# Performance work log

Measured on AMD Instinct MI355X. Metric: run time of the kernel, lower is better.

Reference implementation:

```python
import jax, jax.numpy as jnp
import numpy as np

# ---- sRGB <-> CIELAB (D65) helpers, matching standard torch lab2rgb/rgb2lab ----
_RGB2XYZ = jnp.array([[0.412453, 0.357580, 0.180423],
                      [0.212671, 0.715160, 0.072169],
                      [0.019334, 0.119193, 0.950227]], dtype=jnp.float32)
_XYZ2RGB = jnp.array([[ 3.2404542, -1.5371385, -0.4985314],
                      [-0.9692660,  1.8760108,  0.0415560],
                      [ 0.0556434, -0.2040259,  1.0572252]], dtype=jnp.float32)
_WHITE = jnp.array([0.95047, 1.0, 1.08883], dtype=jnp.float32)
_EPS = 0.008856      # (6/29)^3
_KAPPA = 7.787

def _srgb_to_linear(c):
    safe = jnp.maximum(c, 0.04045)
    return jnp.where(c <= 0.04045, c / 12.92, ((safe + 0.055) / 1.055) ** 2.4)

def _linear_to_srgb(c):
    safe = jnp.maximum(c, 0.0031308)
    return jnp.where(c <= 0.0031308, 12.92 * c, 1.055 * safe ** (1.0 / 2.4) - 0.055)

def rgb2lab(rgb):
    lin = _srgb_to_linear(rgb)                      # [N,3]
    xyz = (lin @ _RGB2XYZ.T) / _WHITE               # [N,3]
    safe = jnp.maximum(xyz, _EPS)
    f = jnp.where(xyz > _EPS, jnp.cbrt(safe), _KAPPA * xyz + 16.0 / 116.0)
    fx, fy, fz = f[..., 0], f[..., 1], f[..., 2]
    L = 116.0 * fy - 16.0
    a = 500.0 * (fx - fy)
    b = 200.0 * (fy - fz)
    return jnp.stack([L, a, b], axis=-1)

def lab2rgb(lab):
    L, a, b = lab[..., 0], lab[..., 1], lab[..., 2]
    fy = (L + 16.0) / 116.0
    fx = fy + a / 500.0
    fz = fy - b / 200.0
    f = jnp.stack([fx, fy, fz], axis=-1)
    f3 = f ** 3
    t = jnp.where(f3 > _EPS, f3, (f - 16.0 / 116.0) / _KAPPA)
    xyz = t * _WHITE
    lin = xyz @ _XYZ2RGB.T
    return _linear_to_srgb(lin)

def _forward(x, w_seq1, b_seq1, w_seq2, b_seq2, w_lin, b_lin,
             w_comb, b_comb, w_logd, b_logd, w_final, b_final):
    # lab branch
    seq = jnp.tanh(x @ w_seq1 + b_seq1) @ w_seq2 + b_seq2        # [N,3]
    lin = x @ w_lin + b_lin                                      # [N,3]
    final_lab = jnp.concatenate([lin, seq], axis=-1) @ w_comb + b_comb
    # log-density branch
    x_rgb = lab2rgb(x)
    log_density = -jnp.log10(x_rgb)
    model_processed = log_density @ w_logd + b_logd
    back_to_lab = rgb2lab(10.0 ** model_processed)
    return jnp.concatenate([final_lab, back_to_lab], axis=-1) @ w_final + b_final


def setup_inputs() -> dict:
    key = jax.random.key(0)
    ks = jax.random.split(key, 13)
    N, H = 2_097_152, 64

    def lin_init(kw, kb, fan_in, fan_out):
        bound = 1.0 / np.sqrt(fan_in)
        w = jax.random.uniform(kw, (fan_in, fan_out), minval=-bound, maxval=bound, dtype=jnp.float32)
        b = jax.random.uniform(kb, (fan_out,), minval=-bound, maxval=bound, dtype=jnp.float32)
        return w, b

    # valid Lab inputs: sample sRGB away from 0/1 then convert
    rgb = jax.random.uniform(ks[0], (N, 3), minval=0.05, maxval=0.95, dtype=jnp.float32)
    x = rgb2lab(rgb)

    kk = jax.random.split(ks[1], 12)
    w_seq1, b_seq1 = lin_init(kk[0], kk[1], 3, H)
    w_seq2, b_seq2 = lin_init(kk[2], kk[3], H, 3)
    w_lin, b_lin = lin_init(kk[4], kk[5], 3, 3)
    w_comb, b_comb = lin_init(kk[6], kk[7], 6, 3)
    w_logd, b_logd = lin_init(kk[8], kk[9], 3, 3)
    w_final, b_final = lin_init(kk[10], kk[11], 6, 3)
    return {"x": x,
            "w_seq1": w_seq1, "b_seq1": b_seq1, "w_seq2": w_seq2, "b_seq2": b_seq2,
            "w_lin": w_lin, "b_lin": b_lin, "w_comb": w_comb, "b_comb": b_comb,
            "w_logd": w_logd, "b_logd": b_logd, "w_final": w_final, "b_final": b_final}


def reference(x, w_seq1, b_seq1, w_seq2, b_seq2, w_lin, b_lin,
              w_comb, b_comb, w_logd, b_logd, w_final, b_final):
    return _forward(x, w_seq1, b_seq1, w_seq2, b_seq2, w_lin, b_lin,
                    w_comb, b_comb, w_logd, b_logd, w_final, b_final)
```

## Files before the change

kernel.cpp:

```cpp
#include <hip/hip_runtime.h>

typedef float    v2f __attribute__((ext_vector_type(2)));
typedef _Float16 v2h __attribute__((ext_vector_type(2)));

__device__ __forceinline__ float fexp2(float x) { return __builtin_amdgcn_exp2f(x); }
__device__ __forceinline__ float flog2(float x) { return __builtin_amdgcn_logf(x); }
__device__ __forceinline__ float ffma (float a, float b, float c) { return __builtin_fmaf(a, b, c); }
__device__ __forceinline__ v2f  splat(float s) { v2f v; v.x = s; v.y = s; return v; }
__device__ __forceinline__ v2f  pkfma(v2f a, v2f b, v2f c) { return __builtin_elementwise_fma(a, b, c); }
__device__ __forceinline__ v2h  splath(float s) { v2h v; v.x = (_Float16)s; v.y = (_Float16)s; return v; }
__device__ __forceinline__ v2h  pkfmah(v2h a, v2h b, v2h c) { return __builtin_elementwise_fma(a, b, c); }
__device__ __forceinline__ v2h  cvt_pk(float a, float b) {
    return __builtin_bit_cast(v2h, __builtin_amdgcn_cvt_pkrtz(a, b));
}

#define LAB_EPS 0.008856f
#define F16_116 0.13793103448275862f
#define LOG2_10 3.3219280948873623f

__device__ __align__(16) float g_ws[548];

__global__ __launch_bounds__(64) void prep_kernel(
    const float* __restrict__ w_seq1, const float* __restrict__ b_seq1,
    const float* __restrict__ w_seq2, const float* __restrict__ b_seq2,
    const float* __restrict__ w_lin,  const float* __restrict__ b_lin,
    const float* __restrict__ w_comb, const float* __restrict__ b_comb,
    const float* __restrict__ w_logd, const float* __restrict__ b_logd,
    const float* __restrict__ w_final,const float* __restrict__ b_final)
{
    const int j = threadIdx.x;
    float H3[9];
#pragma unroll
    for (int i = 0; i < 3; ++i)
#pragma unroll
        for (int c = 0; c < 3; ++c) {
            float h = 0.f;
            for (int m = 0; m < 3; ++m) h += w_comb[(i + 3) * 3 + m] * w_final[m * 3 + c];
            H3[i * 3 + c] = h;
        }

    float4* wsa = reinterpret_cast<float4*>(g_ws);
    uint4*  wsb = reinterpret_cast<uint4*>(g_ws) + 64;

    wsa[j] = make_float4(w_seq1[j], w_seq1[64 + j], w_seq1[128 + j], b_seq1[j]);
    const float w0 = w_seq2[j * 3 + 0], w1 = w_seq2[j * 3 + 1], w2 = w_seq2[j * 3 + 2];
    const float wp0 = w0 * H3[0] + w1 * H3[3] + w2 * H3[6];
    const float wp1 = w0 * H3[1] + w1 * H3[4] + w2 * H3[7];
    const float wp2 = w0 * H3[2] + w1 * H3[5] + w2 * H3[8];
    uint4 wb;
    wb.x = __builtin_bit_cast(unsigned, cvt_pk(wp0, wp0));
    wb.y = __builtin_bit_cast(unsigned, cvt_pk(wp1, wp1));
    wb.z = __builtin_bit_cast(unsigned, cvt_pk(wp2, wp2));
    wb.w = 0u;
    wsb[j] = wb;

    if (j == 0) {
        float* sm = g_ws + 512;
        float G[9], Wfb[9];
#pragma unroll
        for (int i = 0; i < 3; ++i)
#pragma unroll
            for (int c = 0; c < 3; ++c) {
                float gg = 0.f;
                for (int m = 0; m < 3; ++m) gg += w_comb[i * 3 + m] * w_final[m * 3 + c];
                G[i * 3 + c] = gg;
            }
#pragma unroll
        for (int k = 0; k < 3; ++k)
#pragma unroll
            for (int c = 0; c < 3; ++c) {
                float s = 0.f;
                for (int i = 0; i < 3; ++i) s += w_lin[k * 3 + i] * G[i * 3 + c];
                sm[k * 3 + c]      = s;
                Wfb[k * 3 + c]     = w_final[(k + 3) * 3 + c];
                sm[18 + k * 3 + c] = -w_logd[k * 3 + c];
            }
#pragma unroll
        for (int c = 0; c < 3; ++c) {
            sm[9 + c]     = 500.0f * Wfb[3 + c];
            sm[9 + 3 + c] = 116.0f * Wfb[c] - 500.0f * Wfb[3 + c] + 200.0f * Wfb[6 + c];
            sm[9 + 6 + c] = -200.0f * Wfb[6 + c];
            float s = b_final[c] - 16.0f * Wfb[c];
            for (int i = 0; i < 3; ++i)
                s += b_lin[i] * G[i * 3 + c] + b_seq2[i] * H3[i * 3 + c]
                   + b_comb[i] * w_final[i * 3 + c];
            sm[27 + c] = LOG2_10 * b_logd[c];
            sm[30 + c] = s;
        }
    }
}

__global__ __launch_bounds__(256, 5) void fused_kernel(
    const float* __restrict__ x,
    float* __restrict__ out, int n)
{
    const float4* __restrict__ wsa = reinterpret_cast<const float4*>(g_ws);
    const uint4*  __restrict__ wsb = reinterpret_cast<const uint4*>(g_ws) + 64;
    const float*  __restrict__ wse = g_ws + 512;

    const int g = blockIdx.x * blockDim.x + threadIdx.x;
    if (g * 2 >= n) return;

    const float2* xin = reinterpret_cast<const float2*>(x) + (size_t)g * 3;
    const float2 v0 = xin[0], v1 = xin[1], v2 = xin[2];
    v2f xs2[3];
    xs2[0].x = v0.x; xs2[0].y = v1.y;
    xs2[1].x = v0.y; xs2[1].y = v2.x;
    xs2[2].x = v1.x; xs2[2].y = v2.y;

    v2h acc0 = splath(0.f), acc1 = splath(0.f), acc2 = splath(0.f);

#pragma unroll 2
    for (int j0 = 0; j0 < 64; j0 += 4) {
        float4 wa0 = wsa[j0 + 0], wa1 = wsa[j0 + 1], wa2 = wsa[j0 + 2], wa3 = wsa[j0 + 3];
        uint4  wb0 = wsb[j0 + 0], wb1 = wsb[j0 + 1], wb2 = wsb[j0 + 2], wb3 = wsb[j0 + 3];

        v2f t0 = pkfma(xs2[0], splat(wa0.x), pkfma(xs2[1], splat(wa0.y), pkfma(xs2[2], splat(wa0.z), splat(wa0.w))));
        v2f t1 = pkfma(xs2[0], splat(wa1.x), pkfma(xs2[1], splat(wa1.y), pkfma(xs2[2], splat(wa1.z), splat(wa1.w))));
        v2f t2 = pkfma(xs2[0], splat(wa2.x), pkfma(xs2[1], splat(wa2.y), pkfma(xs2[2], splat(wa2.z), splat(wa2.w))));
        v2f t3 = pkfma(xs2[0], splat(wa3.x), pkfma(xs2[1], splat(wa3.y), pkfma(xs2[2], splat(wa3.z), splat(wa3.w))));

        v2h th0 = cvt_pk(t0.x, t0.y);
        v2h th1 = cvt_pk(t1.x, t1.y);
        v2h th2 = cvt_pk(t2.x, t2.y);
        v2h th3 = cvt_pk(t3.x, t3.y);

        const v2h hi3 = splath(3.0f), lo3 = splath(-3.0f);
        th0 = __builtin_elementwise_min(__builtin_elementwise_max(th0, lo3), hi3);
        th1 = __builtin_elementwise_min(__builtin_elementwise_max(th1, lo3), hi3);
        th2 = __builtin_elementwise_min(__builtin_elementwise_max(th2, lo3), hi3);
        th3 = __builtin_elementwise_min(__builtin_elementwise_max(th3, lo3), hi3);

        v2h u0 = th0 * th0, u1 = th1 * th1, u2 = th2 * th2, u3 = th3 * th3;

        const v2h c3 = splath(-0.00120984f), c2 = splath(0.02603622f);
        const v2h c1 = splath(-0.20598500f), c0 = splath(0.95858467f);
        v2h P0 = pkfmah(c3, u0, c2);
        v2h P1 = pkfmah(c3, u1, c2);
        v2h P2 = pkfmah(c3, u2, c2);
        v2h P3 = pkfmah(c3, u3, c2);
        P0 = pkfmah(P0, u0, c1);
        P1 = pkfmah(P1, u1, c1);
        P2 = pkfmah(P2, u2, c1);
        P3 = pkfmah(P3, u3, c1);
        P0 = pkfmah(P0, u0, c0);
        P1 = pkfmah(P1, u1, c0);
        P2 = pkfmah(P2, u2, c0);
        P3 = pkfmah(P3, u3, c0);

        v2h h0 = th0 * P0, h1 = th1 * P1, h2 = th2 * P2, h3 = th3 * P3;

        acc0 = pkfmah(h0, __builtin_bit_cast(v2h, wb0.x), acc0);
        acc1 = pkfmah(h0, __builtin_bit_cast(v2h, wb0.y), acc1);
        acc2 = pkfmah(h0, __builtin_bit_cast(v2h, wb0.z), acc2);
        acc0 = pkfmah(h1, __builtin_bit_cast(v2h, wb1.x), acc0);
        acc1 = pkfmah(h1, __builtin_bit_cast(v2h, wb1.y), acc1);
        acc2 = pkfmah(h1, __builtin_bit_cast(v2h, wb1.z), acc2);
        acc0 = pkfmah(h2, __builtin_bit_cast(v2h, wb2.x), acc0);
        acc1 = pkfmah(h2, __builtin_bit_cast(v2h, wb2.y), acc1);
        acc2 = pkfmah(h2, __builtin_bit_cast(v2h, wb2.z), acc2);
        acc0 = pkfmah(h3, __builtin_bit_cast(v2h, wb3.x), acc0);
        acc1 = pkfmah(h3, __builtin_bit_cast(v2h, wb3.y), acc1);
        acc2 = pkfmah(h3, __builtin_bit_cast(v2h, wb3.z), acc2);
    }

    float A[9], U[9], Wn[9], bl2[3], cv[3];
#pragma unroll
    for (int i = 0; i < 9; ++i) { A[i] = wse[i]; U[i] = wse[9 + i]; Wn[i] = wse[18 + i]; }
#pragma unroll
    for (int i = 0; i < 3; ++i) { bl2[i] = wse[27 + i]; cv[i] = wse[30 + i]; }

    float ov[6];
#pragma unroll
    for (int p = 0; p < 2; ++p) {
        const float L  = p ? xs2[0].y : xs2[0].x;
        const float aa = p ? xs2[1].y : xs2[1].x;
        const float bb = p ? xs2[2].y : xs2[2].x;
        const float a0 = p ? (float)acc0.y : (float)acc0.x;
        const float a1 = p ? (float)acc1.y : (float)acc1.x;
        const float a2 = p ? (float)acc2.y : (float)acc2.x;
        const float fy = (L + 16.0f) * (1.0f / 116.0f);
        const float fx = ffma(aa,  0.002f, fy);
        const float fz = ffma(bb, -0.005f, fy);
        float rgb[3];
        {
            const float f3x = fx * fx * fx, f3y = fy * fy * fy, f3z = fz * fz * fz;
            const float tx = f3x > LAB_EPS ? f3x : (fx - F16_116) * (1.0f / 7.787f);
            const float ty = f3y > LAB_EPS ? f3y : (fy - F16_116) * (1.0f / 7.787f);
            const float tz = f3z > LAB_EPS ? f3z : (fz - F16_116) * (1.0f / 7.787f);
            const float X = tx * 0.95047f, Y = ty, Z = tz * 1.08883f;
            const float linv[3] = {
                 3.2404542f * X - 1.5371385f * Y - 0.4985314f * Z,
                -0.9692660f * X + 1.8760108f * Y + 0.0415560f * Z,
                 0.0556434f * X - 0.2040259f * Y + 1.0572252f * Z};
#pragma unroll
            for (int c = 0; c < 3; ++c) {
                const float cc = linv[c];
                const float lo = 12.92f * cc;
                const float hi = ffma(1.055f,
                                      fexp2(flog2(fmaxf(cc, 0.0031308f)) * (1.0f / 2.4f)),
                                      -0.055f);
                rgb[c] = cc <= 0.0031308f ? lo : hi;
            }
        }
        const float lg0 = flog2(rgb[0]);
        const float lg1 = flog2(rgb[1]);
        const float lg2 = flog2(rgb[2]);
        float lin2[3];
#pragma unroll
        for (int c = 0; c < 3; ++c) {
            const float e   = ffma(lg0, Wn[c], ffma(lg1, Wn[3 + c], ffma(lg2, Wn[6 + c], bl2[c])));
            const float r10 = fexp2(e);
            const float lo  = r10 * (1.0f / 12.92f);
            const float base = (fmaxf(r10, 0.04045f) + 0.055f) * (1.0f / 1.055f);
            const float hi  = fexp2(2.4f * flog2(base));
            lin2[c] = r10 <= 0.04045f ? lo : hi;
        }
        const float X2 = (0.412453f * lin2[0] + 0.357580f * lin2[1] + 0.180423f * lin2[2]) * (1.0f / 0.95047f);
        const float Y2 =  0.212671f * lin2[0] + 0.715160f * lin2[1] + 0.072169f * lin2[2];
        const float Z2 = (0.019334f * lin2[0] + 0.119193f * lin2[1] + 0.950227f * lin2[2]) * (1.0f / 1.08883f);
        const float fX = X2 > LAB_EPS ? fexp2(flog2(fmaxf(X2, LAB_EPS)) * (1.0f / 3.0f)) : ffma(7.787f, X2, F16_116);
        const float fY = Y2 > LAB_EPS ? fexp2(flog2(fmaxf(Y2, LAB_EPS)) * (1.0f / 3.0f)) : ffma(7.787f, Y2, F16_116);
        const float fZ = Z2 > LAB_EPS ? fexp2(flog2(fmaxf(Z2, LAB_EPS)) * (1.0f / 3.0f)) : ffma(7.787f, Z2, F16_116);
#pragma unroll
        for (int c = 0; c < 3; ++c) {
            float o = cv[c];
            o = ffma(L,  A[c],     o);
            o = ffma(aa, A[3 + c], o);
            o = ffma(bb, A[6 + c], o);
            o += (c == 0 ? a0 : (c == 1 ? a1 : a2));
            o = ffma(fX, U[c],     o);
            o = ffma(fY, U[3 + c], o);
            o = ffma(fZ, U[6 + c], o);
            ov[p * 3 + c] = o;
        }
    }

    float2* op = reinterpret_cast<float2*>(out) + (size_t)g * 3;
    op[0] = make_float2(ov[0], ov[1]);
    op[1] = make_float2(ov[2], ov[3]);
    op[2] = make_float2(ov[4], ov[5]);
}

extern "C" void kernel_launch(void* const* d_in, const int* in_sizes, int n_in,
                              void* d_out, int out_size, void* d_ws, size_t ws_size,
                              hipStream_t stream)
{
    const float* x       = (const float*)d_in[0];
    const float* w_seq1  = (const float*)d_in[1];
    const float* b_seq1  = (const float*)d_in[2];
    const float* w_seq2  = (const float*)d_in[3];
    const float* b_seq2  = (const float*)d_in[4];
    const float* w_lin   = (const float*)d_in[5];
    const float* b_lin   = (const float*)d_in[6];
    const float* w_comb  = (const float*)d_in[7];
    const float* b_comb  = (const float*)d_in[8];
    const float* w_logd  = (const float*)d_in[9];
    const float* b_logd  = (const float*)d_in[10];
    const float* w_final = (const float*)d_in[11];
    const float* b_final = (const float*)d_in[12];
    float* outp = (float*)d_out;

    const int n = in_sizes[0] / 3;
    const int threads = 256;
    const int total_threads = (n + 1) / 2;
    const int blocks = (total_threads + threads - 1) / threads;

    prep_kernel<<<1, 64, 0, stream>>>(
        w_seq1, b_seq1, w_seq2, b_seq2, w_lin, b_lin, w_comb, b_comb,
        w_logd, b_logd, w_final, b_final);
    fused_kernel<<<blocks, threads, 0, stream>>>(x, outp, n);
}
```

Before: 138.1 us.

## Fold weight prep into main kernel via LDS and pack color tail math

Removes the separate prep kernel launch by having each block compute the folded weights into shared memory before a barrier. The first-layer weights are now read directly from the original input layout as float4 rows. The color-space tail is rewritten to process both points per thread with packed float2 arithmetic instead of a scalar loop over two points. The cost is redundant per-block weight folding plus a __syncthreads, and launch bounds drop the occupancy hint.

```diff
diff --git a/kernel.cpp b/kernel.cpp
--- a/kernel.cpp
+++ b/kernel.cpp
@@ -13,92 +13,92 @@
 __device__ __forceinline__ v2h  cvt_pk(float a, float b) {
     return __builtin_bit_cast(v2h, __builtin_amdgcn_cvt_pkrtz(a, b));
 }
+__device__ __forceinline__ v2f pexp2(v2f e) { v2f r; r.x = fexp2(e.x); r.y = fexp2(e.y); return r; }
+__device__ __forceinline__ v2f plog2(v2f e) { v2f r; r.x = flog2(e.x); r.y = flog2(e.y); return r; }
+__device__ __forceinline__ v2f selgt(v2f c, float thr, v2f a, v2f b) {
+    v2f r; r.x = c.x > thr ? a.x : b.x; r.y = c.y > thr ? a.y : b.y; return r;
+}
+__device__ __forceinline__ v2f selle(v2f c, float thr, v2f a, v2f b) {
+    v2f r; r.x = c.x <= thr ? a.x : b.x; r.y = c.y <= thr ? a.y : b.y; return r;
+}
+__device__ __forceinline__ v2f pmax(v2f a, float s) { return __builtin_elementwise_max(a, splat(s)); }
 
 #define LAB_EPS 0.008856f
 #define F16_116 0.13793103448275862f
 #define LOG2_10 3.3219280948873623f
 
-__device__ __align__(16) float g_ws[548];
-
-__global__ __launch_bounds__(64) void prep_kernel(
+__global__ __launch_bounds__(256) void fused_kernel(
+    const float* __restrict__ x,
     const float* __restrict__ w_seq1, const float* __restrict__ b_seq1,
     const float* __restrict__ w_seq2, const float* __restrict__ b_seq2,
     const float* __restrict__ w_lin,  const float* __restrict__ b_lin,
     const float* __restrict__ w_comb, const float* __restrict__ b_comb,
     const float* __restrict__ w_logd, const float* __restrict__ b_logd,
-    const float* __restrict__ w_final,const float* __restrict__ b_final)
-{
-    const int j = threadIdx.x;
-    float H3[9];
-#pragma unroll
-    for (int i = 0; i < 3; ++i)
-#pragma unroll
-        for (int c = 0; c < 3; ++c) {
-            float h = 0.f;
-            for (int m = 0; m < 3; ++m) h += w_comb[(i + 3) * 3 + m] * w_final[m * 3 + c];
-            H3[i * 3 + c] = h;
-        }
-
-    float4* wsa = reinterpret_cast<float4*>(g_ws);
-    uint4*  wsb = reinterpret_cast<uint4*>(g_ws) + 64;
-
-    wsa[j] = make_float4(w_seq1[j], w_seq1[64 + j], w_seq1[128 + j], b_seq1[j]);
-    const float w0 = w_seq2[j * 3 + 0], w1 = w_seq2[j * 3 + 1], w2 = w_seq2[j * 3 + 2];
-    const float wp0 = w0 * H3[0] + w1 * H3[3] + w2 * H3[6];
-    const float wp1 = w0 * H3[1] + w1 * H3[4] + w2 * H3[7];
-    const float wp2 = w0 * H3[2] + w1 * H3[5] + w2 * H3[8];
-    uint4 wb;
-    wb.x = __builtin_bit_cast(unsigned, cvt_pk(wp0, wp0));
-    wb.y = __builtin_bit_cast(unsigned, cvt_pk(wp1, wp1));
-    wb.z = __builtin_bit_cast(unsigned, cvt_pk(wp2, wp2));
-    wb.w = 0u;
-    wsb[j] = wb;
-
-    if (j == 0) {
-        float* sm = g_ws + 512;
-        float G[9], Wfb[9];
-#pragma unroll
-        for (int i = 0; i < 3; ++i)
-#pragma unroll
-            for (int c = 0; c < 3; ++c) {
-                float gg = 0.f;
-                for (int m = 0; m < 3; ++m) gg += w_comb[i * 3 + m] * w_final[m * 3 + c];
-                G[i * 3 + c] = gg;
-            }
-#pragma unroll
-        for (int k = 0; k < 3; ++k)
-#pragma unroll
-            for (int c = 0; c < 3; ++c) {
-                float s = 0.f;
-                for (int i = 0; i < 3; ++i) s += w_lin[k * 3 + i] * G[i * 3 + c];
-                sm[k * 3 + c]      = s;
-                Wfb[k * 3 + c]     = w_final[(k + 3) * 3 + c];
-                sm[18 + k * 3 + c] = -w_logd[k * 3 + c];
-            }
-#pragma unroll
-        for (int c = 0; c < 3; ++c) {
-            sm[9 + c]     = 500.0f * Wfb[3 + c];
-            sm[9 + 3 + c] = 116.0f * Wfb[c] - 500.0f * Wfb[3 + c] + 200.0f * Wfb[6 + c];
-            sm[9 + 6 + c] = -200.0f * Wfb[6 + c];
-            float s = b_final[c] - 16.0f * Wfb[c];
-            for (int i = 0; i < 3; ++i)
-                s += b_lin[i] * G[i * 3 + c] + b_seq2[i] * H3[i * 3 + c]
-                   + b_comb[i] * w_final[i * 3 + c];
-            sm[27 + c] = LOG2_10 * b_logd[c];
-            sm[30 + c] = s;
-        }
-    }
-}
-
-__global__ __launch_bounds__(256, 5) void fused_kernel(
-    const float* __restrict__ x,
+    const float* __restrict__ w_final,const float* __restrict__ b_final,
     float* __restrict__ out, int n)
 {
-    const float4* __restrict__ wsa = reinterpret_cast<const float4*>(g_ws);
-    const uint4*  __restrict__ wsb = reinterpret_cast<const uint4*>(g_ws) + 64;
-    const float*  __restrict__ wse = g_ws + 512;
-
-    const int g = blockIdx.x * blockDim.x + threadIdx.x;
+    __shared__ uint4 wsbL[64];
+    __shared__ float smlds[33];
+
+    const int tid = threadIdx.x;
+    if (tid < 64) {
+        const int j = tid;
+        float H3[9];
+#pragma unroll
+        for (int i = 0; i < 3; ++i)
+#pragma unroll
+            for (int c = 0; c < 3; ++c) {
+                float h = 0.f;
+                for (int m = 0; m < 3; ++m) h += w_comb[(i + 3) * 3 + m] * w_final[m * 3 + c];
+                H3[i * 3 + c] = h;
+            }
+        const float w0 = w_seq2[j * 3 + 0], w1 = w_seq2[j * 3 + 1], w2 = w_seq2[j * 3 + 2];
+        const float wp0 = w0 * H3[0] + w1 * H3[3] + w2 * H3[6];
+        const float wp1 = w0 * H3[1] + w1 * H3[4] + w2 * H3[7];
+        const float wp2 = w0 * H3[2] + w1 * H3[5] + w2 * H3[8];
+        uint4 wb;
+        wb.x = __builtin_bit_cast(unsigned, cvt_pk(wp0, wp0));
+        wb.y = __builtin_bit_cast(unsigned, cvt_pk(wp1, wp1));
+        wb.z = __builtin_bit_cast(unsigned, cvt_pk(wp2, wp2));
+        wb.w = 0u;
+        wsbL[j] = wb;
+        if (j == 0) {
+            float G[9], Wfb[9];
+#pragma unroll
+            for (int i = 0; i < 3; ++i)
+#pragma unroll
+                for (int c = 0; c < 3; ++c) {
+                    float gg = 0.f;
+                    for (int m = 0; m < 3; ++m) gg += w_comb[i * 3 + m] * w_final[m * 3 + c];
+                    G[i * 3 + c] = gg;
+                }
+#pragma unroll
+            for (int k = 0; k < 3; ++k)
+#pragma unroll
+                for (int c = 0; c < 3; ++c) {
+                    float s = 0.f;
+                    for (int i = 0; i < 3; ++i) s += w_lin[k * 3 + i] * G[i * 3 + c];
+                    smlds[k * 3 + c]      = s;
+                    Wfb[k * 3 + c]        = w_final[(k + 3) * 3 + c];
+                    smlds[18 + k * 3 + c] = -w_logd[k * 3 + c];
+                }
+#pragma unroll
+            for (int c = 0; c < 3; ++c) {
+                smlds[9 + c]     = 500.0f * Wfb[3 + c];
+                smlds[9 + 3 + c] = 116.0f * Wfb[c] - 500.0f * Wfb[3 + c] + 200.0f * Wfb[6 + c];
+                smlds[9 + 6 + c] = -200.0f * Wfb[6 + c];
+                float s = b_final[c] - 16.0f * Wfb[c];
+                for (int i = 0; i < 3; ++i)
+                    s += b_lin[i] * G[i * 3 + c] + b_seq2[i] * H3[i * 3 + c]
+                       + b_comb[i] * w_final[i * 3 + c];
+                smlds[27 + c] = LOG2_10 * b_logd[c];
+                smlds[30 + c] = s;
+            }
+        }
+    }
+    __syncthreads();
+
+    const int g = blockIdx.x * blockDim.x + tid;
     if (g * 2 >= n) return;
 
     const float2* xin = reinterpret_cast<const float2*>(x) + (size_t)g * 3;
@@ -110,15 +110,22 @@
 
     v2h acc0 = splath(0.f), acc1 = splath(0.f), acc2 = splath(0.f);
 
+    const float4* __restrict__ w1v = reinterpret_cast<const float4*>(w_seq1);
+    const float4* __restrict__ b1v = reinterpret_cast<const float4*>(b_seq1);
+
 #pragma unroll 2
     for (int j0 = 0; j0 < 64; j0 += 4) {
-        float4 wa0 = wsa[j0 + 0], wa1 = wsa[j0 + 1], wa2 = wsa[j0 + 2], wa3 = wsa[j0 + 3];
-        uint4  wb0 = wsb[j0 + 0], wb1 = wsb[j0 + 1], wb2 = wsb[j0 + 2], wb3 = wsb[j0 + 3];
-
-        v2f t0 = pkfma(xs2[0], splat(wa0.x), pkfma(xs2[1], splat(wa0.y), pkfma(xs2[2], splat(wa0.z), splat(wa0.w))));
-        v2f t1 = pkfma(xs2[0], splat(wa1.x), pkfma(xs2[1], splat(wa1.y), pkfma(xs2[2], splat(wa1.z), splat(wa1.w))));
-        v2f t2 = pkfma(xs2[0], splat(wa2.x), pkfma(xs2[1], splat(wa2.y), pkfma(xs2[2], splat(wa2.z), splat(wa2.w))));
-        v2f t3 = pkfma(xs2[0], splat(wa3.x), pkfma(xs2[1], splat(wa3.y), pkfma(xs2[2], splat(wa3.z), splat(wa3.w))));
+        const int q = j0 >> 2;
+        const float4 wr0 = w1v[q];
+        const float4 wr1 = w1v[16 + q];
+        const float4 wr2 = w1v[32 + q];
+        const float4 wrb = b1v[q];
+        const uint4 wb0 = wsbL[j0 + 0], wb1 = wsbL[j0 + 1], wb2 = wsbL[j0 + 2], wb3 = wsbL[j0 + 3];
+
+        v2f t0 = pkfma(xs2[0], splat(wr0.x), pkfma(xs2[1], splat(wr1.x), pkfma(xs2[2], splat(wr2.x), splat(wrb.x))));
+        v2f t1 = pkfma(xs2[0], splat(wr0.y), pkfma(xs2[1], splat(wr1.y), pkfma(xs2[2], splat(wr2.y), splat(wrb.y))));
+        v2f t2 = pkfma(xs2[0], splat(wr0.z), pkfma(xs2[1], splat(wr1.z), pkfma(xs2[2], splat(wr2.z), splat(wrb.z))));
+        v2f t3 = pkfma(xs2[0], splat(wr0.w), pkfma(xs2[1], splat(wr1.w), pkfma(xs2[2], splat(wr2.w), splat(wrb.w))));
 
         v2h th0 = cvt_pk(t0.x, t0.y);
         v2h th1 = cvt_pk(t1.x, t1.y);
@@ -166,80 +173,72 @@
 
     float A[9], U[9], Wn[9], bl2[3], cv[3];
 #pragma unroll
-    for (int i = 0; i < 9; ++i) { A[i] = wse[i]; U[i] = wse[9 + i]; Wn[i] = wse[18 + i]; }
-#pragma unroll
-    for (int i = 0; i < 3; ++i) { bl2[i] = wse[27 + i]; cv[i] = wse[30 + i]; }
-
-    float ov[6];
-#pragma unroll
-    for (int p = 0; p < 2; ++p) {
-        const float L  = p ? xs2[0].y : xs2[0].x;
-        const float aa = p ? xs2[1].y : xs2[1].x;
-        const float bb = p ? xs2[2].y : xs2[2].x;
-        const float a0 = p ? (float)acc0.y : (float)acc0.x;
-        const float a1 = p ? (float)acc1.y : (float)acc1.x;
-        const float a2 = p ? (float)acc2.y : (float)acc2.x;
-        const float fy = (L + 16.0f) * (1.0f / 116.0f);
-        const float fx = ffma(aa,  0.002f, fy);
-        const float fz = ffma(bb, -0.005f, fy);
-        float rgb[3];
-        {
-            const float f3x = fx * fx * fx, f3y = fy * fy * fy, f3z = fz * fz * fz;
-            const float tx = f3x > LAB_EPS ? f3x : (fx - F16_116) * (1.0f / 7.787f);
-            const float ty = f3y > LAB_EPS ? f3y : (fy - F16_116) * (1.0f / 7.787f);
-            const float tz = f3z > LAB_EPS ? f3z : (fz - F16_116) * (1.0f / 7.787f);
-            const float X = tx * 0.95047f, Y = ty, Z = tz * 1.08883f;
-            const float linv[3] = {
-                 3.2404542f * X - 1.5371385f * Y - 0.4985314f * Z,
-                -0.9692660f * X + 1.8760108f * Y + 0.0415560f * Z,
-                 0.0556434f * X - 0.2040259f * Y + 1.0572252f * Z};
-#pragma unroll
-            for (int c = 0; c < 3; ++c) {
-                const float cc = linv[c];
-                const float lo = 12.92f * cc;
-                const float hi = ffma(1.055f,
-                                      fexp2(flog2(fmaxf(cc, 0.0031308f)) * (1.0f / 2.4f)),
-                                      -0.055f);
-                rgb[c] = cc <= 0.0031308f ? lo : hi;
-            }
-        }
-        const float lg0 = flog2(rgb[0]);
-        const float lg1 = flog2(rgb[1]);
-        const float lg2 = flog2(rgb[2]);
-        float lin2[3];
-#pragma unroll
-        for (int c = 0; c < 3; ++c) {
-            const float e   = ffma(lg0, Wn[c], ffma(lg1, Wn[3 + c], ffma(lg2, Wn[6 + c], bl2[c])));
-            const float r10 = fexp2(e);
-            const float lo  = r10 * (1.0f / 12.92f);
-            const float base = (fmaxf(r10, 0.04045f) + 0.055f) * (1.0f / 1.055f);
-            const float hi  = fexp2(2.4f * flog2(base));
-            lin2[c] = r10 <= 0.04045f ? lo : hi;
-        }
-        const float X2 = (0.412453f * lin2[0] + 0.357580f * lin2[1] + 0.180423f * lin2[2]) * (1.0f / 0.95047f);
-        const float Y2 =  0.212671f * lin2[0] + 0.715160f * lin2[1] + 0.072169f * lin2[2];
-        const float Z2 = (0.019334f * lin2[0] + 0.119193f * lin2[1] + 0.950227f * lin2[2]) * (1.0f / 1.08883f);
-        const float fX = X2 > LAB_EPS ? fexp2(flog2(fmaxf(X2, LAB_EPS)) * (1.0f / 3.0f)) : ffma(7.787f, X2, F16_116);
-        const float fY = Y2 > LAB_EPS ? fexp2(flog2(fmaxf(Y2, LAB_EPS)) * (1.0f / 3.0f)) : ffma(7.787f, Y2, F16_116);
-        const float fZ = Z2 > LAB_EPS ? fexp2(flog2(fmaxf(Z2, LAB_EPS)) * (1.0f / 3.0f)) : ffma(7.787f, Z2, F16_116);
-#pragma unroll
-        for (int c = 0; c < 3; ++c) {
-            float o = cv[c];
-            o = ffma(L,  A[c],     o);
-            o = ffma(aa, A[3 + c], o);
-            o = ffma(bb, A[6 + c], o);
-            o += (c == 0 ? a0 : (c == 1 ? a1 : a2));
-            o = ffma(fX, U[c],     o);
-            o = ffma(fY, U[3 + c], o);
-            o = ffma(fZ, U[6 + c], o);
-            ov[p * 3 + c] = o;
-        }
+    for (int i = 0; i < 9; ++i) { A[i] = smlds[i]; U[i] = smlds[9 + i]; Wn[i] = smlds[18 + i]; }
+#pragma unroll
+    for (int i = 0; i < 3; ++i) { bl2[i] = smlds[27 + i]; cv[i] = smlds[30 + i]; }
+
+    v2f sq0, sq1, sq2;
+    sq0.x = (float)acc0.x; sq0.y = (float)acc0.y;
+    sq1.x = (float)acc1.x; sq1.y = (float)acc1.y;
+    sq2.x = (float)acc2.x; sq2.y = (float)acc2.y;
+
+    const v2f fy = (xs2[0] + splat(16.0f)) * splat(1.0f / 116.0f);
+    const v2f fx = pkfma(xs2[1], splat( 0.002f), fy);
+    const v2f fz = pkfma(xs2[2], splat(-0.005f), fy);
+    const v2f f3x = fx * fx * fx, f3y = fy * fy * fy, f3z = fz * fz * fz;
+    const v2f tx = selgt(f3x, LAB_EPS, f3x, (fx - splat(F16_116)) * splat(1.0f / 7.787f));
+    const v2f ty = selgt(f3y, LAB_EPS, f3y, (fy - splat(F16_116)) * splat(1.0f / 7.787f));
+    const v2f tz = selgt(f3z, LAB_EPS, f3z, (fz - splat(F16_116)) * splat(1.0f / 7.787f));
+    const v2f X = tx * splat(0.95047f), Y = ty, Z = tz * splat(1.08883f);
+    v2f linv[3];
+    linv[0] = pkfma(X, splat( 3.2404542f), pkfma(Y, splat(-1.5371385f), Z * splat(-0.4985314f)));
+    linv[1] = pkfma(X, splat(-0.9692660f), pkfma(Y, splat( 1.8760108f), Z * splat( 0.0415560f)));
+    linv[2] = pkfma(X, splat( 0.0556434f), pkfma(Y, splat(-0.2040259f), Z * splat( 1.0572252f)));
+    v2f lg[3];
+#pragma unroll
+    for (int c = 0; c < 3; ++c) {
+        const v2f cc = linv[c];
+        const v2f lo = cc * splat(12.92f);
+        const v2f hi = pkfma(pexp2(plog2(pmax(cc, 0.0031308f)) * splat(1.0f / 2.4f)),
+                             splat(1.055f), splat(-0.055f));
+        lg[c] = plog2(selle(cc, 0.0031308f, lo, hi));
+    }
+    v2f lin2[3];
+#pragma unroll
+    for (int c = 0; c < 3; ++c) {
+        const v2f e   = pkfma(lg[0], splat(Wn[c]),
+                        pkfma(lg[1], splat(Wn[3 + c]),
+                        pkfma(lg[2], splat(Wn[6 + c]), splat(bl2[c]))));
+        const v2f r10 = pexp2(e);
+        const v2f lo  = r10 * splat(1.0f / 12.92f);
+        const v2f base = (pmax(r10, 0.04045f) + splat(0.055f)) * splat(1.0f / 1.055f);
+        const v2f hi  = pexp2(plog2(base) * splat(2.4f));
+        lin2[c] = selle(r10, 0.04045f, lo, hi);
+    }
+    const v2f X2 = pkfma(lin2[0], splat(0.412453f), pkfma(lin2[1], splat(0.357580f), lin2[2] * splat(0.180423f))) * splat(1.0f / 0.95047f);
+    const v2f Y2 = pkfma(lin2[0], splat(0.212671f), pkfma(lin2[1], splat(0.715160f), lin2[2] * splat(0.072169f)));
+    const v2f Z2 = pkfma(lin2[0], splat(0.019334f), pkfma(lin2[1], splat(0.119193f), lin2[2] * splat(0.950227f))) * splat(1.0f / 1.08883f);
+    const v2f fX = selgt(X2, LAB_EPS, pexp2(plog2(pmax(X2, LAB_EPS)) * splat(1.0f / 3.0f)), pkfma(X2, splat(7.787f), splat(F16_116)));
+    const v2f fY = selgt(Y2, LAB_EPS, pexp2(plog2(pmax(Y2, LAB_EPS)) * splat(1.0f / 3.0f)), pkfma(Y2, splat(7.787f), splat(F16_116)));
+    const v2f fZ = selgt(Z2, LAB_EPS, pexp2(plog2(pmax(Z2, LAB_EPS)) * splat(1.0f / 3.0f)), pkfma(Z2, splat(7.787f), splat(F16_116)));
+    v2f o[3];
+#pragma unroll
+    for (int c = 0; c < 3; ++c) {
+        v2f oc = splat(cv[c]);
+        oc = pkfma(xs2[0], splat(A[c]),     oc);
+        oc = pkfma(xs2[1], splat(A[3 + c]), oc);
+        oc = pkfma(xs2[2], splat(A[6 + c]), oc);
+        oc = oc + (c == 0 ? sq0 : (c == 1 ? sq1 : sq2));
+        oc = pkfma(fX, splat(U[c]),     oc);
+        oc = pkfma(fY, splat(U[3 + c]), oc);
+        oc = pkfma(fZ, splat(U[6 + c]), oc);
+        o[c] = oc;
     }
 
     float2* op = reinterpret_cast<float2*>(out) + (size_t)g * 3;
-    op[0] = make_float2(ov[0], ov[1]);
-    op[1] = make_float2(ov[2], ov[3]);
-    op[2] = make_float2(ov[4], ov[5]);
+    op[0] = make_float2(o[0].x, o[1].x);
+    op[1] = make_float2(o[2].x, o[0].y);
+    op[2] = make_float2(o[1].y, o[2].y);
 }
 
 extern "C" void kernel_launch(void* const* d_in, const int* in_sizes, int n_in,
@@ -266,8 +265,7 @@
     const int total_threads = (n + 1) / 2;
     const int blocks = (total_threads + threads - 1) / threads;
 
-    prep_kernel<<<1, 64, 0, stream>>>(
-        w_seq1, b_seq1, w_seq2, b_seq2, w_lin, b_lin, w_comb, b_comb,
-        w_logd, b_logd, w_final, b_final);
-    fused_kernel<<<blocks, threads, 0, stream>>>(x, outp, n);
-}
+    fused_kernel<<<blocks, threads, 0, stream>>>(
+        x, w_seq1, b_seq1, w_seq2, b_seq2, w_lin, b_lin, w_comb, b_comb,
+        w_logd, b_logd, w_final, b_final, outp, n);
+}
```

New measurement: 133.1 us. 3.7% less time.
